# Kernel optimization log

Hardware: AMD Instinct MI355X
Metric: run time of the kernel (lower is better)

The kernel has to match this reference:

```python
import jax, jax.numpy as jnp
import numpy as np

H = 4096      # number of hyperedges in the batch
N = 20000     # number of unique member nodes
FIN = 256     # in_features
FOUT = 128    # out_features
DEG = 32      # member nodes per hyperedge -> E = H*DEG incidence pairs


def setup_inputs() -> dict:
    key = jax.random.key(0)
    k1, k2, k3, k4 = jax.random.split(key, 4)
    xavier = 1.414 * np.sqrt(2.0 / (FIN + FOUT))  # gain=1.414 xavier scale
    hedge_embed = jax.random.normal(k1, (H, FIN), jnp.float32)
    node_embed = jax.random.normal(k2, (N, FIN), jnp.float32)
    Wq = jax.random.normal(k3, (FIN, FOUT), jnp.float32) * xavier
    # each hyperedge has exactly DEG member nodes (guarantees no empty softmax row)
    row_idx = jnp.repeat(jnp.arange(H, dtype=jnp.int64), DEG)
    col_idx = jax.random.randint(k4, (H * DEG,), 0, N, dtype=jnp.int64)
    return {"hedge_embed": hedge_embed, "node_embed": node_embed, "Wq": Wq,
            "row_idx": row_idx, "col_idx": col_idx}


def reference(hedge_embed, node_embed, Wq, row_idx, col_idx):
    # Faithful to NodeAttAggregator.compute:
    #   - queries AND keys both use query_weight (value_weight is unused in output)
    #   - mask filled with float64-min (overflows to -inf in fp32), member
    #     positions overwritten by scores, then row softmax
    #   - aggregation multiplies attention with the KEY projections
    q = hedge_embed @ Wq                                  # [H, FOUT]
    k = node_embed @ Wq                                   # [N, FOUT]
    scores = (q @ k.T) / jnp.sqrt(jnp.float32(FOUT))      # [H, N]
    member = jnp.zeros((H, N), dtype=bool).at[row_idx, col_idx].set(True)
    masked = jnp.where(member, scores, -jnp.inf)          # non-members -> -inf
    attn = jax.nn.softmax(masked, axis=1)                 # [H, N]
    out = (attn @ k).T                                    # [FOUT, H]
    return out
```

## Files before the change

kernel.cpp:

```cpp
#include <hip/hip_runtime.h>
#include <hip/hip_bf16.h>
#include <stdint.h>

#define H_EDGES 4096
#define N_NODES 20000
#define FIN 256
#define FOUT 128
#define DEG 32
#define ROWS_TOTAL 24096
#define G1_BLOCKS 377

typedef float f32x4 __attribute__((ext_vector_type(4)));
typedef short s16x8 __attribute__((ext_vector_type(8)));
typedef unsigned short u16;

__device__ __forceinline__ u16 f2bf(float f) {
    return __builtin_bit_cast(u16, __float2bfloat16(f));
}
__device__ __forceinline__ float bf2f(u16 h) {
    unsigned u = ((unsigned)h) << 16;
    return __builtin_bit_cast(float, u);
}

__global__ __launch_bounds__(256)
void g1_gemm(const float* __restrict__ hedge, const float* __restrict__ node,
             const float* __restrict__ Wq, float* __restrict__ qf,
             u16* __restrict__ kb) {
    __shared__ u16 blds[FOUT * FIN];
    const int t = threadIdx.x;
    const int w = t >> 6, l = t & 63;
    const int lr = l & 15, lp = l >> 4;
    const long rb  = (long)blockIdx.x * 64 + w * 16;
    const long row = rb + lr;
    const long arow = row < ROWS_TOTAL ? row : ROWS_TOTAL - 1;
    const float* pa = arow < H_EDGES ? hedge + arow * FIN
                                     : node + (arow - H_EDGES) * FIN;

    f32x4 au[8], av[8];
    #pragma unroll
    for (int ks = 0; ks < 8; ++ks) {
        au[ks] = *(const f32x4*)(pa + ks * 32 + lp * 8);
        av[ks] = *(const f32x4*)(pa + ks * 32 + lp * 8 + 4);
    }

    {
        const int col   = t >> 1;
        const int sbase = (t & 1) * 16;
        #pragma unroll
        for (int j = 0; j < 16; ++j) {
            const int s  = sbase + j;
            const int k0 = s * 8;
            s16x8 b;
            #pragma unroll
            for (int e = 0; e < 8; ++e)
                b[e] = (short)f2bf(Wq[(size_t)(k0 + e) * FOUT + col]);
            *(s16x8*)(blds + (size_t)(col * 32 + (s ^ (col & 7))) * 8) = b;
        }
    }
    __syncthreads();

    f32x4 acc[8];
    #pragma unroll
    for (int j = 0; j < 8; ++j) acc[j] = (f32x4){0.f, 0.f, 0.f, 0.f};

    #pragma unroll
    for (int ks = 0; ks < 8; ++ks) {
        s16x8 a;
        #pragma unroll
        for (int j = 0; j < 4; ++j) {
            a[j]     = (short)f2bf(au[ks][j]);
            a[j + 4] = (short)f2bf(av[ks][j]);
        }
        #pragma unroll
        for (int cf = 0; cf < 8; ++cf) {
            const int col = cf * 16 + lr;
            s16x8 b = *(const s16x8*)(blds +
                (size_t)(col * 32 + ((ks * 4 + lp) ^ (col & 7))) * 8);
            acc[cf] = __builtin_amdgcn_mfma_f32_16x16x32_bf16(a, b, acc[cf], 0, 0, 0);
        }
    }

    if (rb < H_EDGES) {
        #pragma unroll
        for (int i = 0; i < 4; ++i) {
            const long gr = rb + lp * 4 + i;
            #pragma unroll
            for (int cf = 0; cf < 8; ++cf)
                qf[gr * FOUT + cf * 16 + lr] = acc[cf][i];
        }
    } else {
        #pragma unroll
        for (int i = 0; i < 4; ++i) {
            const long gr = rb + lp * 4 + i;
            if (gr < ROWS_TOTAL) {
                #pragma unroll
                for (int cf = 0; cf < 8; ++cf)
                    kb[(gr - H_EDGES) * FOUT + cf * 16 + lr] = f2bf(acc[cf][i]);
            }
        }
    }
}

__global__ __launch_bounds__(256)
void g2_attn(const float* __restrict__ qf, const u16* __restrict__ kb,
             const int* __restrict__ col_idx, float* __restrict__ out) {
    __shared__ __align__(16) char smem[37888];
    const int t = threadIdx.x;
    const int w = t >> 6, l = t & 63;
    const int e = blockIdx.x * 4 + w;

    char* base = smem + w * 9472;
    u16 (*k_l)[136] = (u16(*)[136])base;
    float* q_l = (float*)(base + 8704);
    float* w_l = q_l + 128;
    int*   c_l = (int*)(w_l + 32);

    if (l < DEG) c_l[l] = col_idx[(size_t)e * DEG + l];
    q_l[l]      = qf[(size_t)e * FOUT + l];
    q_l[l + 64] = qf[(size_t)e * FOUT + 64 + l];
    __syncthreads();

    #pragma unroll
    for (int it = 0; it < 8; ++it) {
        const int s = l + 64 * it;
        const int m = s >> 4, sl = s & 15;
        *(s16x8*)&k_l[m][sl * 8] =
            *(const s16x8*)(kb + (size_t)c_l[m] * FOUT + sl * 8);
    }
    __syncthreads();

    const int m = l >> 1, he = l & 1;
    float p = 0.f;
    #pragma unroll
    for (int j = 0; j < 8; ++j) {
        s16x8 kv = *(const s16x8*)&k_l[m][he * 64 + j * 8];
        #pragma unroll
        for (int ee = 0; ee < 8; ++ee)
            p = fmaf(q_l[he * 64 + j * 8 + ee], bf2f((u16)kv[ee]), p);
    }
    p += __shfl_xor(p, 1);
    const float sc = p * 0.08838834764831845f;

    const int cm = c_l[m];
    bool valid = true;
    for (int j = 0; j < m; ++j)
        if (c_l[j] == cm) valid = false;
    const float sv = valid ? sc : -INFINITY;
    float mx = sv;
    #pragma unroll
    for (int d = 1; d < 64; d <<= 1) mx = fmaxf(mx, __shfl_xor(mx, d));
    const float ex = valid ? __expf(sv - mx) : 0.f;
    float sum = ex;
    #pragma unroll
    for (int d = 1; d < 64; d <<= 1) sum += __shfl_xor(sum, d);
    if (he == 0) w_l[m] = ex * 2.f / sum;
    __syncthreads();

    float a0 = 0.f, a1 = 0.f;
    #pragma unroll
    for (int mm = 0; mm < DEG; ++mm) {
        const float wv = w_l[mm];
        a0 = fmaf(wv, bf2f(k_l[mm][l]), a0);
        a1 = fmaf(wv, bf2f(k_l[mm][l + 64]), a1);
    }
    __syncthreads();

    float (*tile)[4] = (float(*)[4])smem;
    tile[l][w]      = a0;
    tile[l + 64][w] = a1;
    __syncthreads();
    if (t < FOUT) {
        f32x4 v = *(const f32x4*)tile[t];
        *(f32x4*)(out + (size_t)t * H_EDGES + blockIdx.x * 4) = v;
    }
}

extern "C" void kernel_launch(void* const* d_in, const int* in_sizes, int n_in,
                              void* d_out, int out_size, void* d_ws, size_t ws_size,
                              hipStream_t stream) {
    const float* hedge   = (const float*)d_in[0];
    const float* node    = (const float*)d_in[1];
    const float* Wq      = (const float*)d_in[2];
    const int*   col_idx = (const int*)d_in[4];
    float* out = (float*)d_out;

    char* ws = (char*)d_ws;
    float* qf = (float*)ws;
    u16*   kb = (u16*)(ws + (size_t)H_EDGES * FOUT * 4);

    g1_gemm<<<G1_BLOCKS, 256, 0, stream>>>(hedge, node, Wq, qf, kb);
    g2_attn<<<H_EDGES / 4, 256, 0, stream>>>(qf, kb, col_idx, out);
}
```

Measured before the change: 36.00 us.

## Pre-convert Wq to swizzled bf16 once and drop intra-wave barriers in attention

Adds a small prep kernel that converts Wq to bf16 and writes it in the swizzled LDS layout, so each of the 377 GEMM blocks does a straight coalesced vector copy instead of strided fp32 gathers and per-element conversion. In the attention kernel, the per-wave key tile moves to an XOR-swizzled layout to reduce bank conflicts, and block-wide barriers are removed because each wave only touches its own shared region. The cost is an extra kernel launch and workspace buffer, and it depends on wave-local LDS visibility without explicit barriers.

```diff
diff --git a/kernel.cpp b/kernel.cpp
--- a/kernel.cpp
+++ b/kernel.cpp
@@ -23,8 +23,34 @@
 }
 
 __global__ __launch_bounds__(256)
+void k0_prep(const float* __restrict__ Wq, u16* __restrict__ bt) {
+    __shared__ u16 lt[32][72];
+    const int t  = threadIdx.x;
+    const int kt = blockIdx.x >> 2;
+    const int ct = blockIdx.x & 3;
+    const int k0 = kt * 64, c0 = ct * 32;
+
+    #pragma unroll
+    for (int p = 0; p < 2; ++p) {
+        const int r = p * 32 + (t >> 3);
+        const int q = t & 7;
+        f32x4 v = *(const f32x4*)(Wq + (size_t)(k0 + r) * FOUT + c0 + q * 4);
+        #pragma unroll
+        for (int j = 0; j < 4; ++j) lt[q * 4 + j][r] = f2bf(v[j]);
+    }
+    __syncthreads();
+
+    const int cl = t >> 3;
+    const int sl = t & 7;
+    const int col = c0 + cl;
+    const int s_glob = kt * 8 + sl;
+    const int phys = s_glob ^ (col & 7);
+    *(s16x8*)(bt + (size_t)(col * 32 + phys) * 8) = *(const s16x8*)&lt[cl][sl * 8];
+}
+
+__global__ __launch_bounds__(256)
 void g1_gemm(const float* __restrict__ hedge, const float* __restrict__ node,
-             const float* __restrict__ Wq, float* __restrict__ qf,
+             const u16* __restrict__ bt, float* __restrict__ qf,
              u16* __restrict__ kb) {
     __shared__ u16 blds[FOUT * FIN];
     const int t = threadIdx.x;
@@ -44,18 +70,10 @@
     }
 
     {
-        const int col   = t >> 1;
-        const int sbase = (t & 1) * 16;
-        #pragma unroll
-        for (int j = 0; j < 16; ++j) {
-            const int s  = sbase + j;
-            const int k0 = s * 8;
-            s16x8 b;
-            #pragma unroll
-            for (int e = 0; e < 8; ++e)
-                b[e] = (short)f2bf(Wq[(size_t)(k0 + e) * FOUT + col]);
-            *(s16x8*)(blds + (size_t)(col * 32 + (s ^ (col & 7))) * 8) = b;
-        }
+        const s16x8* src = (const s16x8*)bt;
+        s16x8* dst = (s16x8*)blds;
+        #pragma unroll
+        for (int j = 0; j < 16; ++j) { const int s = t + 256 * j; dst[s] = src[s]; }
     }
     __syncthreads();
 
@@ -109,31 +127,32 @@
     const int w = t >> 6, l = t & 63;
     const int e = blockIdx.x * 4 + w;
 
-    char* base = smem + w * 9472;
-    u16 (*k_l)[136] = (u16(*)[136])base;
-    float* q_l = (float*)(base + 8704);
+    float (*tile)[4] = (float(*)[4])smem;
+    char* base = smem + 2048 + w * 8960;
+    u16*   kl  = (u16*)base;
+    float* q_l = (float*)(base + 8192);
     float* w_l = q_l + 128;
     int*   c_l = (int*)(w_l + 32);
 
     if (l < DEG) c_l[l] = col_idx[(size_t)e * DEG + l];
     q_l[l]      = qf[(size_t)e * FOUT + l];
     q_l[l + 64] = qf[(size_t)e * FOUT + 64 + l];
-    __syncthreads();
 
     #pragma unroll
     for (int it = 0; it < 8; ++it) {
         const int s = l + 64 * it;
         const int m = s >> 4, sl = s & 15;
-        *(s16x8*)&k_l[m][sl * 8] =
+        const int phys = m * 16 + (sl & 8) + ((sl & 7) ^ (m & 7));
+        *(s16x8*)(kl + (size_t)phys * 8) =
             *(const s16x8*)(kb + (size_t)c_l[m] * FOUT + sl * 8);
     }
-    __syncthreads();
 
     const int m = l >> 1, he = l & 1;
     float p = 0.f;
     #pragma unroll
     for (int j = 0; j < 8; ++j) {
-        s16x8 kv = *(const s16x8*)&k_l[m][he * 64 + j * 8];
+        const int phys = m * 16 + he * 8 + (j ^ (m & 7));
+        s16x8 kv = *(const s16x8*)(kl + (size_t)phys * 8);
         #pragma unroll
         for (int ee = 0; ee < 8; ++ee)
             p = fmaf(q_l[he * 64 + j * 8 + ee], bf2f((u16)kv[ee]), p);
@@ -154,18 +173,17 @@
     #pragma unroll
     for (int d = 1; d < 64; d <<= 1) sum += __shfl_xor(sum, d);
     if (he == 0) w_l[m] = ex * 2.f / sum;
-    __syncthreads();
-
+
+    const int sl0 = l >> 3, el = l & 7;
     float a0 = 0.f, a1 = 0.f;
     #pragma unroll
     for (int mm = 0; mm < DEG; ++mm) {
         const float wv = w_l[mm];
-        a0 = fmaf(wv, bf2f(k_l[mm][l]), a0);
-        a1 = fmaf(wv, bf2f(k_l[mm][l + 64]), a1);
-    }
-    __syncthreads();
-
-    float (*tile)[4] = (float(*)[4])smem;
+        const int p0 = mm * 16 + (sl0 ^ (mm & 7));
+        a0 = fmaf(wv, bf2f(kl[(size_t)p0 * 8 + el]), a0);
+        a1 = fmaf(wv, bf2f(kl[(size_t)(p0 + 8) * 8 + el]), a1);
+    }
+
     tile[l][w]      = a0;
     tile[l + 64][w] = a1;
     __syncthreads();
@@ -187,7 +205,10 @@
     char* ws = (char*)d_ws;
     float* qf = (float*)ws;
     u16*   kb = (u16*)(ws + (size_t)H_EDGES * FOUT * 4);
-
-    g1_gemm<<<G1_BLOCKS, 256, 0, stream>>>(hedge, node, Wq, qf, kb);
+    u16*   bt = (u16*)(ws + (size_t)H_EDGES * FOUT * 4
+                          + (size_t)N_NODES * FOUT * 2);
+
+    k0_prep<<<16, 256, 0, stream>>>(Wq, bt);
+    g1_gemm<<<G1_BLOCKS, 256, 0, stream>>>(hedge, node, bt, qf, kb);
     g2_attn<<<H_EDGES / 4, 256, 0, stream>>>(qf, kb, col_idx, out);
 }
```

New measurement: 31.28 us. 1.15x faster.
